# Kernel optimization log

Measured on AMD Instinct MI355X. Metric: run time of the kernel, lower is better.

The kernel has to match this reference:

```python
import jax, jax.numpy as jnp
import numpy as np

# Faithful notes on the original torch code:
# - MLP path with n_networks=1: angles = MLP(coeffs), shape [N,1]. Dropout is
#   eval-mode identity (dropout=0.0).
# - aggregate_k_hop: step_k is a single buffer that torch_scatter ACCUMULATES into
#   across hops (scatter(..., out=step_k) adds into out), and enhanced_angles
#   ALIASES angles, so `enhanced_angles += step_k` mutates the angle vector that
#   is read at the next hop. We reproduce both behaviors.
# - k-hop paths are deduplicated via np.unique, i.e. the scatter at hop k sums
#   angles[dest] over UNIQUE (src,dest) pairs reachable in exactly k edge steps.
#   That is exactly the boolean k-th power of the adjacency matrix, so we use
#   dense boolean matrix powers (static shapes, jit-friendly) instead of the
#   dynamic-shape unique() roundtrip.

N_NODES = 4096
IN_DIM = 128
N_EDGES = 131072
K_HOPS = 3


def setup_inputs() -> dict:
    key = jax.random.key(0)
    ks = jax.random.split(key, 8)
    coeffs = jax.random.normal(ks[0], (N_NODES, IN_DIM), dtype=jnp.float32)
    edge_index = jax.random.randint(ks[1], (2, N_EDGES), 0, N_NODES, dtype=jnp.int64)
    # Xavier-normal linear weights (torch layout: [out, in])
    def xavier(k, out_d, in_d):
        std = np.sqrt(2.0 / (in_d + out_d)).astype(np.float32)
        return jax.random.normal(k, (out_d, in_d), dtype=jnp.float32) * std
    W0 = xavier(ks[2], IN_DIM, IN_DIM)
    b0 = jnp.zeros((IN_DIM,), jnp.float32)
    W1 = xavier(ks[3], IN_DIM, IN_DIM)  # use_bias=False
    W2 = xavier(ks[4], IN_DIM, IN_DIM)
    W3 = xavier(ks[5], 1, IN_DIM)
    b3 = jnp.zeros((1,), jnp.float32)
    return {"coeffs": coeffs, "edge_index": edge_index,
            "W0": W0, "b0": b0, "W1": W1, "W2": W2, "W3": W3, "b3": b3}


def reference(coeffs, edge_index, W0, b0, W1, W2, W3, b3):
    n = coeffs.shape[0]
    h = jax.nn.relu(coeffs @ W0.T + b0)
    h = jax.nn.relu(h @ W1.T)
    h = jax.nn.relu(h @ W2.T)
    a = h @ W3.T + b3  # [N, 1]

    # ---- aggregate_k_hop (k=3), f(k) = log(k+1) ----
    row, col = edge_index[0], edge_index[1]
    # hop 1: raw edge list scatter (duplicates kept, as in the original)
    step = jax.ops.segment_sum(a[col] * jnp.float32(np.log(2.0)), row,
                               num_segments=n)  # [N,1]
    a = a + step
    # hops >= 2: unique k-step paths == boolean adjacency power
    A = jnp.zeros((n, n), jnp.bool_).at[row, col].set(True)
    Af = A.astype(jnp.float32)
    Ak = Af
    for k_ in range(2, K_HOPS + 1):
        Ak = ((Ak @ Af) > 0).astype(jnp.float32)  # unique k_-hop reachability
        step = step + jnp.float32(np.log(k_ + 1.0)) * (Ak @ a)
        a = a + step
    return a
```

## Files before the change

### kernel.cpp

```cpp
#include <hip/hip_runtime.h>
#include <cstdint>
#include <cstddef>


constexpr int NN   = 4096;
constexpr int D    = 128;
constexpr int NE   = 131072;
constexpr int WPR  = 64;
constexpr int MAXN = 256;

typedef __attribute__((ext_vector_type(8))) short  short8;
typedef __attribute__((ext_vector_type(4))) float  float4v;

__device__ __forceinline__ unsigned short f32_bf16(float x) {
  unsigned u = __float_as_uint(x);
  return (unsigned short)((u + 0x7FFFu + ((u >> 16) & 1u)) >> 16);
}
__device__ __forceinline__ float bf16_f32(unsigned short b) {
  return __uint_as_float(((unsigned)b) << 16);
}

struct Frag { short8 hi; short8 lo; };

__device__ __forceinline__ Frag split8(const float* __restrict__ p) {
  float4v a = *(const float4v*)p;
  float4v b = *(const float4v*)(p + 4);
  Frag f;
#pragma unroll
  for (int j = 0; j < 4; ++j) {
    float x = a[j];
    unsigned short h = f32_bf16(x);
    f.hi[j] = (short)h;
    f.lo[j] = (short)f32_bf16(x - bf16_f32(h));
    float y = b[j];
    unsigned short h2 = f32_bf16(y);
    f.hi[j + 4] = (short)h2;
    f.lo[j + 4] = (short)f32_bf16(y - bf16_f32(h2));
  }
  return f;
}

__device__ __forceinline__ float4v mfma4(const Frag& A, const Frag& B, float4v c) {
  c = __builtin_amdgcn_mfma_f32_16x16x32_bf16(A.lo, B.lo, c, 0, 0, 0);
  c = __builtin_amdgcn_mfma_f32_16x16x32_bf16(A.lo, B.hi, c, 0, 0, 0);
  c = __builtin_amdgcn_mfma_f32_16x16x32_bf16(A.hi, B.lo, c, 0, 0, 0);
  c = __builtin_amdgcn_mfma_f32_16x16x32_bf16(A.hi, B.hi, c, 0, 0, 0);
  return c;
}

__device__ __forceinline__ float wave_sum64(float v) {
#pragma unroll
  for (int off = 32; off >= 1; off >>= 1) v += __shfl_xor(v, off, 64);
  return v;
}

__global__ __launch_bounds__(256) void mlp_mfma(
    const float* __restrict__ coeffs,
    const float* __restrict__ W0, const float* __restrict__ b0,
    const float* __restrict__ W1, const float* __restrict__ W2,
    const float* __restrict__ W3, const float* __restrict__ b3,
    float* __restrict__ a0v,
    unsigned long long* __restrict__ A, float* __restrict__ s1,
    float* __restrict__ ws2) {
  __shared__ float hbuf[16 * 132];
  __shared__ float psh[4][16];
  const int b = blockIdx.x, t = threadIdx.x;
  const int wave = t >> 6, lane = t & 63;
  const int quad = lane >> 4, l16 = lane & 15;
  const int node0 = b * 16;
  const int ot0 = 2 * wave, ot1 = 2 * wave + 1;

  {
    float4v z4 = {0.f, 0.f, 0.f, 0.f};
    float4v* Az = (float4v*)A + (size_t)b * 512;
    Az[t] = z4;
    Az[t + 256] = z4;
    if (t < 4) ((float4v*)(s1 + node0))[t] = z4;
    if (b == 0 && t < 16) ((float4v*)ws2)[t] = z4;
  }

  const float* Wsrc[3] = {W0, W1, W2};
  float4v r0, r1;
#pragma unroll
  for (int L = 0; L < 3; ++L) {
    Frag Af[4];
    const float* abase = (L == 0)
        ? coeffs + (size_t)(node0 + l16) * D + quad * 8
        : hbuf + l16 * 132 + quad * 8;
#pragma unroll
    for (int kt = 0; kt < 4; ++kt) Af[kt] = split8(abase + kt * 32);
    const float* Wb = Wsrc[L];
    float4v acc0 = {0.f, 0.f, 0.f, 0.f}, acc1 = acc0;
#pragma unroll
    for (int kt = 0; kt < 4; ++kt) {
      Frag B0 = split8(Wb + (size_t)(ot0 * 16 + l16) * D + kt * 32 + quad * 8);
      Frag B1 = split8(Wb + (size_t)(ot1 * 16 + l16) * D + kt * 32 + quad * 8);
      acc0 = mfma4(Af[kt], B0, acc0);
      acc1 = mfma4(Af[kt], B1, acc1);
    }
    if (L == 0) {
      float ba = b0[ot0 * 16 + l16], bb = b0[ot1 * 16 + l16];
#pragma unroll
      for (int j = 0; j < 4; ++j) { acc0[j] += ba; acc1[j] += bb; }
    }
#pragma unroll
    for (int j = 0; j < 4; ++j) {
      acc0[j] = fmaxf(acc0[j], 0.f);
      acc1[j] = fmaxf(acc1[j], 0.f);
    }
    if (L < 2) {
      __syncthreads();
#pragma unroll
      for (int j = 0; j < 4; ++j) {
        hbuf[(quad * 4 + j) * 132 + ot0 * 16 + l16] = acc0[j];
        hbuf[(quad * 4 + j) * 132 + ot1 * 16 + l16] = acc1[j];
      }
      __syncthreads();
    } else {
      r0 = acc0; r1 = acc1;
    }
  }
  float w3a = W3[ot0 * 16 + l16], w3b = W3[ot1 * 16 + l16];
#pragma unroll
  for (int j = 0; j < 4; ++j) {
    float v = fmaf(r0[j], w3a, r1[j] * w3b);
#pragma unroll
    for (int off = 1; off <= 8; off <<= 1) v += __shfl_xor(v, off, 64);
    if (l16 == 0) psh[wave][quad * 4 + j] = v;
  }
  __syncthreads();
  if (t < 16)
    a0v[node0 + t] = psh[0][t] + psh[1][t] + psh[2][t] + psh[3][t] + b3[0];
}

__global__ __launch_bounds__(256) void build_graph(
    const int* __restrict__ er, const int* __restrict__ ec,
    const float* __restrict__ a0, unsigned long long* __restrict__ A,
    float* __restrict__ s1) {
  int e = blockIdx.x * 256 + threadIdx.x;
  if (e >= NE) return;
  int r = er[e] & (NN - 1);
  int c = ec[e] & (NN - 1);
  atomicOr(&A[(size_t)r * WPR + (c >> 6)], 1ull << (c & 63));
  atomicAdd(&s1[r], a0[c] * 0.6931471805599453f);
}

__global__ __launch_bounds__(256) void a1_ws(
    const float* __restrict__ a0, const float* __restrict__ s1,
    float* __restrict__ a1, float* __restrict__ ws1) {
  int t = threadIdx.x, i = blockIdx.x * 256 + t;
  float v = a0[i] + s1[i];
  a1[i] = v;
  float s = wave_sum64(v);
  if ((t & 63) == 0) ws1[i >> 6] = s;
}

__device__ __forceinline__ void stage_v(const float* __restrict__ v,
                                        float* __restrict__ vl, int t) {
#pragma unroll
  for (int u = 0; u < 16; ++u) {
    int j = t + u * 256;
    vl[(j >> 6) * 65 + (j & 63)] = v[j];
  }
}

__device__ __forceinline__ unsigned long long gather_row(
    const unsigned long long* __restrict__ Arow,
    const unsigned long long* __restrict__ SRC,
    int i, int lane, unsigned short* __restrict__ nbr, int* __restrict__ ncnt) {
  if (lane == 0) *ncnt = 0;
  unsigned long long rw = Arow[(size_t)i * WPR + lane];
  int c = __popcll(rw);
  int base = 0;
  if (c) base = atomicAdd(ncnt, c);
  while (rw) {
    int b = __builtin_ctzll(rw);
    rw &= rw - 1ull;
    if (base < MAXN) nbr[base] = (unsigned short)((lane << 6) + b);
    ++base;
  }
  int cnt = *ncnt;
  cnt = cnt < MAXN ? cnt : MAXN;
  unsigned long long acc = 0ull;
  int j = 0;
  for (; j + 8 <= cnt; j += 8) {
    unsigned long long v0 = SRC[(size_t)nbr[j + 0] * WPR + lane];
    unsigned long long v1 = SRC[(size_t)nbr[j + 1] * WPR + lane];
    unsigned long long v2 = SRC[(size_t)nbr[j + 2] * WPR + lane];
    unsigned long long v3 = SRC[(size_t)nbr[j + 3] * WPR + lane];
    unsigned long long v4 = SRC[(size_t)nbr[j + 4] * WPR + lane];
    unsigned long long v5 = SRC[(size_t)nbr[j + 5] * WPR + lane];
    unsigned long long v6 = SRC[(size_t)nbr[j + 6] * WPR + lane];
    unsigned long long v7 = SRC[(size_t)nbr[j + 7] * WPR + lane];
    acc |= ((v0 | v1) | (v2 | v3)) | ((v4 | v5) | (v6 | v7));
  }
  for (; j < cnt; ++j) acc |= SRC[(size_t)nbr[j] * WPR + lane];
  return acc;
}

__device__ __forceinline__ float masked_dot(
    unsigned long long m, const float* __restrict__ vl,
    const float* __restrict__ wsum, int lane) {
  int cnt = __popcll(m);
  bool inv = cnt > 32;
  unsigned long long it = inv ? ~m : m;
  float part = inv ? wsum[lane] : 0.f;
  float sgn = inv ? -1.f : 1.f;
  const float* p = vl + lane * 65;
  float acc = 0.f;
  while (it) {
    int b = __builtin_ctzll(it);
    it &= it - 1ull;
    acc += p[b];
  }
  return fmaf(sgn, acc, part);
}

__global__ __launch_bounds__(256) void hop2(
    const unsigned long long* __restrict__ A, unsigned long long* __restrict__ A2,
    const float* __restrict__ a1, const float* __restrict__ ws1,
    const float* __restrict__ s1, float* __restrict__ s2, float* __restrict__ a2,
    float* __restrict__ ws2) {
  __shared__ float vl[64 * 65];
  __shared__ unsigned short nbr[4][MAXN];
  __shared__ int ncnt[4];
  int t = threadIdx.x, wave = t >> 6, lane = t & 63;
  stage_v(a1, vl, t);
  __syncthreads();
  int i = blockIdx.x * 4 + wave;
  unsigned long long acc = gather_row(A, A, i, lane, nbr[wave], &ncnt[wave]);
  A2[(size_t)i * WPR + lane] = acc;
  float part = masked_dot(acc, vl, ws1, lane);
  part = wave_sum64(part);
  if (lane == 0) {
    float s2v = fmaf(1.0986122886681098f, part, s1[i]);
    s2[i] = s2v;
    float a2v = a1[i] + s2v;
    a2[i] = a2v;
    atomicAdd(&ws2[i >> 6], a2v);
  }
}

__global__ __launch_bounds__(256) void hop3(
    const unsigned long long* __restrict__ A, const unsigned long long* __restrict__ A2,
    const float* __restrict__ a2, const float* __restrict__ ws2,
    const float* __restrict__ s2, float* __restrict__ out) {
  __shared__ float vl[64 * 65];
  __shared__ unsigned short nbr[4][MAXN];
  __shared__ int ncnt[4];
  int t = threadIdx.x, wave = t >> 6, lane = t & 63;
  stage_v(a2, vl, t);
  __syncthreads();
  int i = blockIdx.x * 4 + wave;
  unsigned long long acc = gather_row(A, A2, i, lane, nbr[wave], &ncnt[wave]);
  float part = masked_dot(acc, vl, ws2, lane);
  part = wave_sum64(part);
  if (lane == 0)
    out[i] = a2[i] + fmaf(1.3862943611198906f, part, s2[i]);
}

extern "C" void kernel_launch(void* const* d_in, const int* in_sizes, int n_in,
                              void* d_out, int out_size, void* d_ws, size_t ws_size,
                              hipStream_t stream) {
  const float* coeffs = (const float*)d_in[0];
  const int*   edge   = (const int*)d_in[1];
  const float* W0 = (const float*)d_in[2];
  const float* b0 = (const float*)d_in[3];
  const float* W1 = (const float*)d_in[4];
  const float* W2 = (const float*)d_in[5];
  const float* W3 = (const float*)d_in[6];
  const float* b3 = (const float*)d_in[7];
  float* out = (float*)d_out;

  char* ws = (char*)d_ws;
  unsigned long long* A  = (unsigned long long*)ws;
  unsigned long long* A2 = (unsigned long long*)(ws + (2u << 20));
  float* f   = (float*)(ws + (4u << 20));
  float* a0v = f;
  float* a1v = f + 4096;
  float* s1  = f + 8192;
  float* s2  = f + 12288;
  float* a2v = f + 16384;
  float* ws1 = f + 20480;
  float* ws2 = f + 20544;

  mlp_mfma<<<NN / 16, 256, 0, stream>>>(coeffs, W0, b0, W1, W2, W3, b3,
                                        a0v, A, s1, ws2);
  build_graph<<<NE / 256, 256, 0, stream>>>(edge, edge + NE, a0v, A, s1);
  a1_ws<<<NN / 256, 256, 0, stream>>>(a0v, s1, a1v, ws1);
  hop2<<<NN / 4, 256, 0, stream>>>(A, A2, a1v, ws1, s1, s2, a2v, ws2);
  hop3<<<NN / 4, 256, 0, stream>>>(A, A2, a2v, ws2, s2, out);
}
```

Baseline: 140.8 us.

## Prepack MLP weights into bf16 hi/lo fragments and halve nodes per block

```diff
diff --git a/kernel.cpp b/kernel.cpp
--- a/kernel.cpp
+++ b/kernel.cpp
@@ -40,8 +40,7 @@
   return f;
 }
 
-__device__ __forceinline__ float4v mfma4(const Frag& A, const Frag& B, float4v c) {
-  c = __builtin_amdgcn_mfma_f32_16x16x32_bf16(A.lo, B.lo, c, 0, 0, 0);
+__device__ __forceinline__ float4v mfma3(const Frag& A, const Frag& B, float4v c) {
   c = __builtin_amdgcn_mfma_f32_16x16x32_bf16(A.lo, B.hi, c, 0, 0, 0);
   c = __builtin_amdgcn_mfma_f32_16x16x32_bf16(A.hi, B.lo, c, 0, 0, 0);
   c = __builtin_amdgcn_mfma_f32_16x16x32_bf16(A.hi, B.hi, c, 0, 0, 0);
@@ -54,10 +53,22 @@
   return v;
 }
 
+__global__ __launch_bounds__(256) void pack_w(
+    const float* __restrict__ W0, const float* __restrict__ W1,
+    const float* __restrict__ W2, short* __restrict__ Wp) {
+  int tid = blockIdx.x * 256 + threadIdx.x;
+  int lane = tid & 63, kt = (tid >> 6) & 3, o = (tid >> 8) & 7, L = tid >> 11;
+  int quad = lane >> 4, l16 = lane & 15;
+  const float* W = (L == 0) ? W0 : (L == 1) ? W1 : W2;
+  Frag f = split8(W + (size_t)(o * 16 + l16) * D + kt * 32 + quad * 8);
+  short* base = Wp + (size_t)(((L * 8 + o) * 4) + kt) * 1024;
+  *(short8*)(base + lane * 8) = f.hi;
+  *(short8*)(base + 512 + lane * 8) = f.lo;
+}
+
 __global__ __launch_bounds__(256) void mlp_mfma(
-    const float* __restrict__ coeffs,
-    const float* __restrict__ W0, const float* __restrict__ b0,
-    const float* __restrict__ W1, const float* __restrict__ W2,
+    const float* __restrict__ coeffs, const short* __restrict__ Wp,
+    const float* __restrict__ b0,
     const float* __restrict__ W3, const float* __restrict__ b3,
     float* __restrict__ a0v,
     unsigned long long* __restrict__ A, float* __restrict__ s1,
@@ -67,36 +78,38 @@
   const int b = blockIdx.x, t = threadIdx.x;
   const int wave = t >> 6, lane = t & 63;
   const int quad = lane >> 4, l16 = lane & 15;
-  const int node0 = b * 16;
+  const int node0 = b * 8;
   const int ot0 = 2 * wave, ot1 = 2 * wave + 1;
 
   {
     float4v z4 = {0.f, 0.f, 0.f, 0.f};
-    float4v* Az = (float4v*)A + (size_t)b * 512;
-    Az[t] = z4;
-    Az[t + 256] = z4;
-    if (t < 4) ((float4v*)(s1 + node0))[t] = z4;
+    ((float4v*)A)[(size_t)b * 256 + t] = z4;
+    if (t < 2) ((float4v*)(s1 + node0))[t] = z4;
     if (b == 0 && t < 16) ((float4v*)ws2)[t] = z4;
   }
 
-  const float* Wsrc[3] = {W0, W1, W2};
   float4v r0, r1;
 #pragma unroll
   for (int L = 0; L < 3; ++L) {
     Frag Af[4];
     const float* abase = (L == 0)
-        ? coeffs + (size_t)(node0 + l16) * D + quad * 8
-        : hbuf + l16 * 132 + quad * 8;
+        ? coeffs + (size_t)(node0 + (l16 & 7)) * D + quad * 8
+        : hbuf + (l16 & 7) * 132 + quad * 8;
 #pragma unroll
     for (int kt = 0; kt < 4; ++kt) Af[kt] = split8(abase + kt * 32);
-    const float* Wb = Wsrc[L];
+    const short* WL = Wp + (size_t)L * 8 * 4 * 1024;
     float4v acc0 = {0.f, 0.f, 0.f, 0.f}, acc1 = acc0;
 #pragma unroll
     for (int kt = 0; kt < 4; ++kt) {
-      Frag B0 = split8(Wb + (size_t)(ot0 * 16 + l16) * D + kt * 32 + quad * 8);
-      Frag B1 = split8(Wb + (size_t)(ot1 * 16 + l16) * D + kt * 32 + quad * 8);
-      acc0 = mfma4(Af[kt], B0, acc0);
-      acc1 = mfma4(Af[kt], B1, acc1);
+      const short* p0 = WL + (size_t)(ot0 * 4 + kt) * 1024 + lane * 8;
+      const short* p1 = WL + (size_t)(ot1 * 4 + kt) * 1024 + lane * 8;
+      Frag B0, B1;
+      B0.hi = *(const short8*)p0;
+      B0.lo = *(const short8*)(p0 + 512);
+      B1.hi = *(const short8*)p1;
+      B1.lo = *(const short8*)(p1 + 512);
+      acc0 = mfma3(Af[kt], B0, acc0);
+      acc1 = mfma3(Af[kt], B1, acc1);
     }
     if (L == 0) {
       float ba = b0[ot0 * 16 + l16], bb = b0[ot1 * 16 + l16];
@@ -129,7 +142,7 @@
     if (l16 == 0) psh[wave][quad * 4 + j] = v;
   }
   __syncthreads();
-  if (t < 16)
+  if (t < 8)
     a0v[node0 + t] = psh[0][t] + psh[1][t] + psh[2][t] + psh[3][t] + b3[0];
 }
 
@@ -283,9 +296,10 @@
   float* a2v = f + 16384;
   float* ws1 = f + 20480;
   float* ws2 = f + 20544;
-
-  mlp_mfma<<<NN / 16, 256, 0, stream>>>(coeffs, W0, b0, W1, W2, W3, b3,
-                                        a0v, A, s1, ws2);
+  short* Wp  = (short*)(ws + (4u << 20) + 128 * 1024);
+
+  pack_w<<<24, 256, 0, stream>>>(W0, W1, W2, Wp);
+  mlp_mfma<<<NN / 8, 256, 0, stream>>>(coeffs, Wp, b0, W3, b3, a0v, A, s1, ws2);
   build_graph<<<NE / 256, 256, 0, stream>>>(edge, edge + NE, a0v, A, s1);
   a1_ws<<<NN / 256, 256, 0, stream>>>(a0v, s1, a1v, ws1);
   hop2<<<NN / 4, 256, 0, stream>>>(A, A2, a1v, ws1, s1, s2, a2v, ws2);
```

Result: no change. 141.6 us (+0.6%).
